# Kernel optimization log

Hardware: AMD Instinct MI355X
Metric: run time of the kernel (lower is better)

The kernel has to match this reference:

```python
import jax, jax.numpy as jnp
import numpy as np

D_MODEL = 512
EPS = 1e-5  # torch LayerNorm default


def _layernorm(x, g, b):
    mu = jnp.mean(x, axis=-1, keepdims=True)
    var = jnp.mean(jnp.square(x - mu), axis=-1, keepdims=True)
    return (x - mu) * jax.lax.rsqrt(var + EPS) * g + b


def setup_inputs() -> dict:
    key = jax.random.key(0)
    ks = jax.random.split(key, 12)
    d = D_MODEL
    s = 1.0 / np.sqrt(d)
    s4 = 1.0 / np.sqrt(4 * d)
    return {
        "x": jax.random.normal(ks[0], (4, 4096, d), dtype=jnp.float32),
        "Wq": jax.random.uniform(ks[1], (d, d), jnp.float32, -s, s),
        "bq": jax.random.uniform(ks[2], (d,), jnp.float32, -s, s),
        "Wk": jax.random.uniform(ks[3], (d, d), jnp.float32, -s, s),
        "bk": jax.random.uniform(ks[4], (d,), jnp.float32, -s, s),
        "Wv": jax.random.uniform(ks[5], (d, d), jnp.float32, -s, s),
        "bv": jax.random.uniform(ks[6], (d,), jnp.float32, -s, s),
        "g1": jnp.ones((d,), jnp.float32),
        "b1": jnp.zeros((d,), jnp.float32),
        "g2": jnp.ones((d,), jnp.float32),
        "b2": jnp.zeros((d,), jnp.float32),
        "W1": jax.random.uniform(ks[7], (d, 4 * d), jnp.float32, -s, s),
        "bf1": jax.random.uniform(ks[8], (4 * d,), jnp.float32, -s, s),
        "W2": jax.random.uniform(ks[9], (4 * d, d), jnp.float32, -s4, s4),
        "bf2": jax.random.uniform(ks[10], (d,), jnp.float32, -s4, s4),
    }


def reference(x, Wq, bq, Wk, bk, Wv, bv, g1, b1, g2, b2, W1, bf1, W2, bf2):
    # QKV projections: [b, s, d]
    Q = jnp.einsum("bsd,de->bse", x, Wq) + bq
    K = jnp.einsum("bsd,de->bse", x, Wk) + bk
    V = jnp.einsum("bsd,de->bse", x, Wv) + bv
    scale = 1.0 / jnp.sqrt(jnp.float32(K.shape[-1]))
    scores = jnp.einsum("bqd,bkd->bqk", Q, K) * scale  # [b, s, s]
    attn = jax.nn.softmax(scores, axis=-1)
    att = jnp.einsum("bqk,bkd->bqd", attn, V)
    x = _layernorm(x + att, g1, b1)
    h = jax.nn.relu(jnp.einsum("bsd,df->bsf", x, W1) + bf1)
    ffn = jnp.einsum("bsf,fd->bsd", h, W2) + bf2
    return _layernorm(x + ffn, g2, b2)
```

## Files before the change

### kernel.cpp

```cpp
#include <hip/hip_runtime.h>
#include <hip/hip_bf16.h>

typedef unsigned short u16;
typedef short bf16x8 __attribute__((ext_vector_type(8)));
typedef float f32x4 __attribute__((ext_vector_type(4)));

__device__ __forceinline__ float b2f(u16 u) {
  union { float f; unsigned int i; } v; v.i = ((unsigned int)u) << 16; return v.f;
}
__device__ __forceinline__ u16 f2b(float f) {
  union { float f; unsigned int i; } v; v.f = f;
  unsigned int r = v.i + 0x7fffu + ((v.i >> 16) & 1u);
  return (u16)(r >> 16);
}
__device__ __forceinline__ u16 to_b(float v) { return f2b(v); }
__device__ __forceinline__ u16 to_b(u16 v) { return v; }
__device__ __forceinline__ float to_f(float v) { return v; }
__device__ __forceinline__ float to_f(u16 v) { return b2f(v); }

__device__ __forceinline__ void gl_lds16(const u16* g, u16* l) {
  __builtin_amdgcn_global_load_lds(
      (const __attribute__((address_space(1))) unsigned int*)g,
      (__attribute__((address_space(3))) unsigned int*)l, 16, 0, 0);
}

template <bool RELU, bool ATOMIC>
__global__ __launch_bounds__(256)
void gemm_nt(const u16* __restrict__ A, const u16* __restrict__ Bt,
             const float* __restrict__ bias, void* __restrict__ Cv,
             int N, int K, int nsplit, int lda, int ldb, int ldc,
             long sA, long sB, long sC, float scale) {
  __shared__ __align__(16) u16 As[128 * 64];
  __shared__ __align__(16) u16 Bs[128 * 64];
  const int z = blockIdx.z;
  const int batch = z / nsplit, split = z - batch * nsplit;
  const int Ks = K / nsplit;
  const u16* Ab = A + (long)batch * sA + (long)split * Ks;
  const u16* Bb = Bt + (long)batch * sB + (long)split * Ks;
  const int m0 = blockIdx.y * 128, n0 = blockIdx.x * 128;
  const int t = threadIdx.x, w = t >> 6, lane = t & 63;
  const int wm = (w >> 1) * 64, wn = (w & 1) * 64;
  const int lr = lane & 15, q = lane >> 4;

  int srow[4], scol[4];
#pragma unroll
  for (int i = 0; i < 4; i++) {
    int n = w * 256 + i * 64 + lane;
    srow[i] = n >> 3;
    scol[i] = (((n & 7) ^ ((n >> 3) & 7)) * 8);
  }

  f32x4 acc[4][4];
#pragma unroll
  for (int i = 0; i < 4; i++)
#pragma unroll
    for (int j = 0; j < 4; j++) acc[i][j] = (f32x4){0.f, 0.f, 0.f, 0.f};

  for (int k0 = 0; k0 < Ks; k0 += 64) {
#pragma unroll
    for (int i = 0; i < 4; i++)
      gl_lds16(Ab + (long)(m0 + srow[i]) * lda + k0 + scol[i], &As[(w * 256 + i * 64) * 8]);
#pragma unroll
    for (int i = 0; i < 4; i++)
      gl_lds16(Bb + (long)(n0 + srow[i]) * ldb + k0 + scol[i], &Bs[(w * 256 + i * 64) * 8]);
    __syncthreads();
#pragma unroll
    for (int kk = 0; kk < 2; kk++) {
      bf16x8 af[4], bfr[4];
#pragma unroll
      for (int i = 0; i < 4; i++) {
        int row = wm + i * 16 + lr;
        af[i] = *(const bf16x8*)&As[row * 64 + (((kk * 4 + q) ^ (row & 7)) * 8)];
      }
#pragma unroll
      for (int j = 0; j < 4; j++) {
        int row = wn + j * 16 + lr;
        bfr[j] = *(const bf16x8*)&Bs[row * 64 + (((kk * 4 + q) ^ (row & 7)) * 8)];
      }
#pragma unroll
      for (int i = 0; i < 4; i++)
#pragma unroll
        for (int j = 0; j < 4; j++)
          acc[i][j] = __builtin_amdgcn_mfma_f32_16x16x32_bf16(af[i], bfr[j], acc[i][j], 0, 0, 0);
    }
    __syncthreads();
  }

#pragma unroll
  for (int j = 0; j < 4; j++) {
    int cg = n0 + wn + j * 16 + lr;
    float bb = (!ATOMIC && bias) ? bias[cg] : 0.0f;
#pragma unroll
    for (int i = 0; i < 4; i++) {
      int rbase = m0 + wm + i * 16 + q * 4;
#pragma unroll
      for (int r = 0; r < 4; r++) {
        float vv = acc[i][j][r] * scale;
        if (ATOMIC) {
          atomicAdd((float*)Cv + (long)batch * sC + (long)(rbase + r) * ldc + cg, vv);
        } else {
          vv += bb;
          if (RELU) vv = fmaxf(vv, 0.0f);
          ((u16*)Cv)[(long)batch * sC + (long)(rbase + r) * ldc + cg] = f2b(vv);
        }
      }
    }
  }
}

#define STAGE_K(kvv, kcc, sel)                                               \
  {                                                                          \
    _Pragma("unroll") for (int rr = 0; rr < 4; rr++)                         \
        gl_lds16(Kbase + (long)((kvv) * 128 + srow[rr]) * 1536 +             \
                     (kcc) * 128 + scol8[rr],                                \
                 &B2[(sel)][ldsd[rr]]);                                      \
  }
#define STAGE_V(kvv, dcc, sel)                                               \
  {                                                                          \
    _Pragma("unroll") for (int rr = 0; rr < 4; rr++)                         \
        gl_lds16(Vtb + (long)((dcc) * 128 + srow[rr]) * 4096 +               \
                     (kvv) * 128 + scol8[rr],                                \
                 &B2[(sel)][ldsd[rr]]);                                      \
  }
#define VMW4()  asm volatile("s_waitcnt vmcnt(4)" ::: "memory")
#define VMW0()  asm volatile("s_waitcnt vmcnt(0)" ::: "memory")
#define CFENCE() asm volatile("" ::: "memory")

__global__ __launch_bounds__(512, 2)
void flash_attn(const u16* __restrict__ QKV, const u16* __restrict__ Vt,
                u16* __restrict__ attp, float* __restrict__ lbp, float scl) {
  __shared__ __align__(16) u16 B2[2][128 * 128];
  __shared__ __align__(16) u16 Pb[128 * 136];
  const int flat = blockIdx.x;
  const int batch = (flat & 7) >> 1, half = flat & 1, qt = flat >> 3;
  const int t = threadIdx.x, w = t >> 6, lane = t & 63;
  const int lr = lane & 15, q = lane >> 4;
  const long rowbase = (long)batch * 4096 + qt * 128;
  const u16* Qrow  = QKV + (rowbase + w * 16 + lr) * 1536;
  const u16* Kbase = QKV + ((long)batch * 4096 + half * 2048) * 1536 + 512;
  const u16* Vtb   = Vt + (long)batch * 512 * 4096 + half * 2048;
  u16* Pw = &Pb[w * (16 * 136)];

  int srow[4], scol8[4], ldsd[4];
#pragma unroll
  for (int rr = 0; rr < 4; rr++) {
    int n = rr * 512 + t;
    srow[rr] = n >> 4;
    scol8[rr] = ((n & 15) ^ ((n >> 4) & 15)) * 8;
    ldsd[rr] = (rr * 512 + w * 64) * 8;
  }

  f32x4 O[32];
#pragma unroll
  for (int i = 0; i < 32; i++) O[i] = (f32x4){0.f, 0.f, 0.f, 0.f};
  float lsum[4] = {0.f, 0.f, 0.f, 0.f};

  STAGE_K(0, 0, 0);
  int par = 0;

  for (int kv = 0; kv < 16; kv++) {
    f32x4 S[8];
#pragma unroll
    for (int j = 0; j < 8; j++) S[j] = (f32x4){0.f, 0.f, 0.f, 0.f};

#pragma unroll
    for (int kc = 0; kc < 4; kc++) {
      if (kc < 3) { STAGE_K(kv, kc + 1, par ^ 1); }
      else        { STAGE_V(kv, 0, par ^ 1); }
      VMW4();
      __builtin_amdgcn_s_barrier();
      CFENCE();
      __builtin_amdgcn_s_setprio(1);
      bf16x8 Qf[4];
#pragma unroll
      for (int ss = 0; ss < 4; ss++)
        Qf[ss] = *(const bf16x8*)(Qrow + kc * 128 + ss * 32 + q * 8);
#pragma unroll
      for (int ss = 0; ss < 4; ss++)
#pragma unroll
        for (int j = 0; j < 8; j++) {
          int row = j * 16 + lr;
          bf16x8 Kf = *(const bf16x8*)&B2[par][row * 128 + (((ss * 4 + q) ^ lr) * 8)];
          S[j] = __builtin_amdgcn_mfma_f32_16x16x32_bf16(Qf[ss], Kf, S[j], 0, 0, 0);
        }
      __builtin_amdgcn_s_setprio(0);
      CFENCE();
      __builtin_amdgcn_s_barrier();
      par ^= 1;
    }

    float psum[4] = {0.f, 0.f, 0.f, 0.f};
#pragma unroll
    for (int j = 0; j < 8; j++)
#pragma unroll
      for (int r = 0; r < 4; r++) {
        float e = __expf(S[j][r] * scl);
        psum[r] += e;
        Pw[(q * 4 + r) * 136 + j * 16 + lr] = f2b(e);
      }
#pragma unroll
    for (int r = 0; r < 4; r++) {
#pragma unroll
      for (int o = 1; o < 16; o <<= 1) psum[r] += __shfl_xor(psum[r], o);
      lsum[r] += psum[r];
    }
    bf16x8 Pf[4];
#pragma unroll
    for (int t4 = 0; t4 < 4; t4++)
      Pf[t4] = *(const bf16x8*)&Pw[lr * 136 + t4 * 32 + q * 8];

#pragma unroll
    for (int dc = 0; dc < 4; dc++) {
      if (dc < 3) {
        STAGE_V(kv, dc + 1, par ^ 1);
        VMW4();
      } else if (kv < 15) {
        STAGE_K(kv + 1, 0, par ^ 1);
        VMW4();
      } else {
        VMW0();
      }
      __builtin_amdgcn_s_barrier();
      CFENCE();
      __builtin_amdgcn_s_setprio(1);
#pragma unroll
      for (int t4 = 0; t4 < 4; t4++)
#pragma unroll
        for (int j = 0; j < 8; j++) {
          int row = j * 16 + lr;
          bf16x8 Vf = *(const bf16x8*)&B2[par][row * 128 + (((t4 * 4 + q) ^ lr) * 8)];
          O[dc * 8 + j] = __builtin_amdgcn_mfma_f32_16x16x32_bf16(Pf[t4], Vf, O[dc * 8 + j], 0, 0, 0);
        }
      __builtin_amdgcn_s_setprio(0);
      CFENCE();
      __builtin_amdgcn_s_barrier();
      par ^= 1;
    }
  }

  u16* op = attp + (long)half * 16384 * 512;
#pragma unroll
  for (int i = 0; i < 32; i++) {
    int col = (i >> 3) * 128 + (i & 7) * 16 + lr;
#pragma unroll
    for (int r = 0; r < 4; r++)
      op[(rowbase + w * 16 + q * 4 + r) * 512 + col] = f2b(O[i][r]);
  }
  if (lr == 0)
#pragma unroll
    for (int r = 0; r < 4; r++)
      lbp[(long)half * 16384 + rowbase + w * 16 + q * 4 + r] = lsum[r];
}

template <typename TS>
__global__ __launch_bounds__(1024)
void transpose_b(const TS* __restrict__ src, u16* __restrict__ dst,
                 int R, int Cc, int src_ld, long sbs, long dbs) {
  __shared__ u16 tile[32][33];
  int r = blockIdx.y * 32 + threadIdx.y;
  int c = blockIdx.x * 32 + threadIdx.x;
  tile[threadIdx.y][threadIdx.x] = to_b(src[(long)blockIdx.z * sbs + (long)r * src_ld + c]);
  __syncthreads();
  int rr = blockIdx.x * 32 + threadIdx.y;
  int cc = blockIdx.y * 32 + threadIdx.x;
  dst[(long)blockIdx.z * dbs + (long)rr * R + cc] = tile[threadIdx.x][threadIdx.y];
}

__global__ __launch_bounds__(256)
void f32_to_bf16(const float* __restrict__ s, u16* __restrict__ d) {
  long i = ((long)blockIdx.x * 256 + threadIdx.x) * 8;
  float4 a0 = *(const float4*)(s + i);
  float4 a1 = *(const float4*)(s + i + 4);
  u16 tmp[8] = {f2b(a0.x), f2b(a0.y), f2b(a0.z), f2b(a0.w),
                f2b(a1.x), f2b(a1.y), f2b(a1.z), f2b(a1.w)};
  *(uint4*)(d + i) = *(uint4*)tmp;
}

__global__ __launch_bounds__(256)
void add_ln_att(const float* __restrict__ X, const u16* __restrict__ attp,
                const float* __restrict__ lbp,
                const float* __restrict__ g, const float* __restrict__ b,
                u16* __restrict__ O) {
  const int row = blockIdx.x * 4 + (threadIdx.x >> 6);
  const int lane = threadIdx.x & 63;
  const size_t base = (size_t)row * 512 + lane * 8;
  const float inv = 1.0f / (lbp[row] + lbp[16384 + row]);
  uint4 p0 = *(const uint4*)(attp + base);
  uint4 p1 = *(const uint4*)(attp + 16384L * 512 + base);
  const u16* s0 = (const u16*)&p0;
  const u16* s1 = (const u16*)&p1;
  float z[8];
  float s1a = 0.f, s2a = 0.f;
#pragma unroll
  for (int i = 0; i < 8; i++) {
    z[i] = X[base + i] + (b2f(s0[i]) + b2f(s1[i])) * inv;
    s1a += z[i]; s2a += z[i] * z[i];
  }
#pragma unroll
  for (int o = 32; o > 0; o >>= 1) { s1a += __shfl_xor(s1a, o); s2a += __shfl_xor(s2a, o); }
  const float mu = s1a * (1.0f / 512.0f);
  const float var = s2a * (1.0f / 512.0f) - mu * mu;
  const float rstd = rsqrtf(var + 1e-5f);
#pragma unroll
  for (int i = 0; i < 8; i++) {
    int c = lane * 8 + i;
    O[base + i] = f2b((z[i] - mu) * rstd * g[c] + b[c]);
  }
}

__global__ __launch_bounds__(256)
void add_ln_ffn(const u16* __restrict__ X, const u16* __restrict__ P0,
                const u16* __restrict__ P1, const float* __restrict__ eb,
                const float* __restrict__ g, const float* __restrict__ b,
                float* __restrict__ O) {
  const int row = blockIdx.x * 4 + (threadIdx.x >> 6);
  const int lane = threadIdx.x & 63;
  const size_t base = (size_t)row * 512 + lane * 8;
  uint4 xv = *(const uint4*)(X + base);
  uint4 a0 = *(const uint4*)(P0 + base);
  uint4 a1 = *(const uint4*)(P1 + base);
  const u16* xs = (const u16*)&xv;
  const u16* s0 = (const u16*)&a0;
  const u16* s1 = (const u16*)&a1;
  float z[8];
  float s1a = 0.f, s2a = 0.f;
#pragma unroll
  for (int i = 0; i < 8; i++) {
    int c = lane * 8 + i;
    z[i] = b2f(xs[i]) + b2f(s0[i]) + b2f(s1[i]) + eb[c];
    s1a += z[i]; s2a += z[i] * z[i];
  }
#pragma unroll
  for (int o = 32; o > 0; o >>= 1) { s1a += __shfl_xor(s1a, o); s2a += __shfl_xor(s2a, o); }
  const float mu = s1a * (1.0f / 512.0f);
  const float var = s2a * (1.0f / 512.0f) - mu * mu;
  const float rstd = rsqrtf(var + 1e-5f);
#pragma unroll
  for (int i = 0; i < 8; i++) {
    int c = lane * 8 + i;
    O[base + i] = (z[i] - mu) * rstd * g[c] + b[c];
  }
}

__global__ __launch_bounds__(256)
void concat3(const float* __restrict__ a, const float* __restrict__ b,
             const float* __restrict__ c, float* __restrict__ o) {
  int i = threadIdx.x + blockIdx.x * 256;
  if (i < 512) o[i] = a[i];
  else if (i < 1024) o[i] = b[i - 512];
  else if (i < 1536) o[i] = c[i - 1024];
}

extern "C" void kernel_launch(void* const* d_in, const int* in_sizes, int n_in,
                              void* d_out, int out_size, void* d_ws, size_t ws_size,
                              hipStream_t stream) {
  const float* x   = (const float*)d_in[0];
  const float* Wq  = (const float*)d_in[1];
  const float* bq  = (const float*)d_in[2];
  const float* Wk  = (const float*)d_in[3];
  const float* bk  = (const float*)d_in[4];
  const float* Wv  = (const float*)d_in[5];
  const float* bv  = (const float*)d_in[6];
  const float* g1  = (const float*)d_in[7];
  const float* b1  = (const float*)d_in[8];
  const float* g2  = (const float*)d_in[9];
  const float* b2  = (const float*)d_in[10];
  const float* W1  = (const float*)d_in[11];
  const float* bf1 = (const float*)d_in[12];
  const float* W2  = (const float*)d_in[13];
  const float* bf2 = (const float*)d_in[14];
  float* out = (float*)d_out;

  char* ws = (char*)d_ws;
  const size_t MB = 1048576;
  u16*   QKV   = (u16*)(ws + 0);
  u16*   Vt    = (u16*)(ws + 48 * MB);
  u16*   attp  = (u16*)(ws + 64 * MB);
  u16*   h     = (u16*)(ws + 64 * MB);
  float* lbp   = (float*)(ws + 128 * MB);
  u16*   x1    = (u16*)(ws + 129 * MB);
  u16*   ffnp  = (u16*)(ws + 145 * MB);
  u16*   xb    = (u16*)(ws + 145 * MB);
  u16*   wqkvt = (u16*)(ws + 177 * MB);
  u16*   w1t   = wqkvt + 1536 * 512;
  u16*   w2t   = w1t + 2048 * 512;
  float* bqkv  = (float*)(w2t + 512 * 2048);

  dim3 tb(32, 32);
  f32_to_bf16<<<4096, 256, 0, stream>>>(x, xb);
  transpose_b<float><<<dim3(16, 16, 1), tb, 0, stream>>>(Wq, wqkvt,              512, 512, 512, 0, 0);
  transpose_b<float><<<dim3(16, 16, 1), tb, 0, stream>>>(Wk, wqkvt + 512 * 512,  512, 512, 512, 0, 0);
  transpose_b<float><<<dim3(16, 16, 1), tb, 0, stream>>>(Wv, wqkvt + 1024 * 512, 512, 512, 512, 0, 0);
  transpose_b<float><<<dim3(64, 16, 1), tb, 0, stream>>>(W1, w1t, 512, 2048, 2048, 0, 0);
  transpose_b<float><<<dim3(16, 64, 1), tb, 0, stream>>>(W2, w2t, 2048, 512, 512, 0, 0);
  concat3<<<6, 256, 0, stream>>>(bq, bk, bv, bqkv);

  gemm_nt<false, false><<<dim3(12, 128, 1), 256, 0, stream>>>(
      xb, wqkvt, bqkv, QKV, 1536, 512, 1, 512, 512, 1536, 0, 0, 0, 1.0f);

  transpose_b<u16><<<dim3(16, 128, 4), tb, 0, stream>>>(
      QKV + 1024, Vt, 4096, 512, 1536, 4096L * 1536, 512L * 4096);

  const float scl = 0.044194173824159216f;
  flash_attn<<<dim3(256, 1, 1), 512, 0, stream>>>(QKV, Vt, attp, lbp, scl);

  add_ln_att<<<4096, 256, 0, stream>>>(x, attp, lbp, g1, b1, x1);
  gemm_nt<true, false><<<dim3(16, 128, 1), 256, 0, stream>>>(
      x1, w1t, bf1, h, 2048, 512, 1, 512, 512, 2048, 0, 0, 0, 1.0f);
  gemm_nt<false, false><<<dim3(4, 128, 2), 256, 0, stream>>>(
      h, w2t, nullptr, ffnp, 512, 1024, 1, 2048, 2048, 512,
      1024, 1024, 16384L * 512, 1.0f);
  add_ln_ffn<<<4096, 256, 0, stream>>>(
      x1, ffnp, ffnp + 16384L * 512, bf2, g2, b2, out);
}
```

Before: 522.1 us.

## Switch flash attention to 32x32x16 MFMA with shared-LDS P tile

The attention kernel moves from 16x16x32 to 32x32x16 bf16 MFMAs. Each wave now owns a 32-row query group and half of the KV or D columns, so operand loads from LDS are reused across a larger output tile. The whole-block P tile is written to LDS with a swizzle and read back after an extra barrier. Row sums are now reduced across 32 lanes and stored as four partials instead of two, and the add+LayerNorm kernel sums all four. The aim is fewer LDS reads per MFMA flop, at the cost of an extra barrier and a larger row-sum buffer.

After: 698.5 us. +33.8%, slower.

```diff
diff --git a/kernel.cpp b/kernel.cpp
--- a/kernel.cpp
+++ b/kernel.cpp
@@ -4,6 +4,7 @@
 typedef unsigned short u16;
 typedef short bf16x8 __attribute__((ext_vector_type(8)));
 typedef float f32x4 __attribute__((ext_vector_type(4)));
+typedef float f32x16 __attribute__((ext_vector_type(16)));
 
 __device__ __forceinline__ float b2f(u16 u) {
   union { float f; unsigned int i; } v; v.i = ((unsigned int)u) << 16; return v.f;
@@ -130,16 +131,16 @@
 void flash_attn(const u16* __restrict__ QKV, const u16* __restrict__ Vt,
                 u16* __restrict__ attp, float* __restrict__ lbp, float scl) {
   __shared__ __align__(16) u16 B2[2][128 * 128];
-  __shared__ __align__(16) u16 Pb[128 * 136];
+  __shared__ __align__(16) u16 Pb[128 * 128];
   const int flat = blockIdx.x;
   const int batch = (flat & 7) >> 1, half = flat & 1, qt = flat >> 3;
   const int t = threadIdx.x, w = t >> 6, lane = t & 63;
-  const int lr = lane & 15, q = lane >> 4;
+  const int rg = w & 3, sh = w >> 2;
+  const int c32 = lane & 31, hi = lane >> 5;
   const long rowbase = (long)batch * 4096 + qt * 128;
-  const u16* Qrow  = QKV + (rowbase + w * 16 + lr) * 1536;
+  const u16* Qp    = QKV + (rowbase + rg * 32 + c32) * 1536;
   const u16* Kbase = QKV + ((long)batch * 4096 + half * 2048) * 1536 + 512;
   const u16* Vtb   = Vt + (long)batch * 512 * 4096 + half * 2048;
-  u16* Pw = &Pb[w * (16 * 136)];
 
   int srow[4], scol8[4], ldsd[4];
 #pragma unroll
@@ -150,18 +151,24 @@
     ldsd[rr] = (rr * 512 + w * 64) * 8;
   }
 
-  f32x4 O[32];
-#pragma unroll
-  for (int i = 0; i < 32; i++) O[i] = (f32x4){0.f, 0.f, 0.f, 0.f};
-  float lsum[4] = {0.f, 0.f, 0.f, 0.f};
+  f32x16 O[8];
+#pragma unroll
+  for (int i = 0; i < 8; i++)
+#pragma unroll
+    for (int r = 0; r < 16; r++) O[i][r] = 0.f;
+  float lsum[16];
+#pragma unroll
+  for (int r = 0; r < 16; r++) lsum[r] = 0.f;
 
   STAGE_K(0, 0, 0);
   int par = 0;
 
   for (int kv = 0; kv < 16; kv++) {
-    f32x4 S[8];
-#pragma unroll
-    for (int j = 0; j < 8; j++) S[j] = (f32x4){0.f, 0.f, 0.f, 0.f};
+    f32x16 S[2];
+#pragma unroll
+    for (int tt = 0; tt < 2; tt++)
+#pragma unroll
+      for (int r = 0; r < 16; r++) S[tt][r] = 0.f;
 
 #pragma unroll
     for (int kc = 0; kc < 4; kc++) {
@@ -171,17 +178,17 @@
       __builtin_amdgcn_s_barrier();
       CFENCE();
       __builtin_amdgcn_s_setprio(1);
-      bf16x8 Qf[4];
-#pragma unroll
-      for (int ss = 0; ss < 4; ss++)
-        Qf[ss] = *(const bf16x8*)(Qrow + kc * 128 + ss * 32 + q * 8);
-#pragma unroll
-      for (int ss = 0; ss < 4; ss++)
-#pragma unroll
-        for (int j = 0; j < 8; j++) {
-          int row = j * 16 + lr;
-          bf16x8 Kf = *(const bf16x8*)&B2[par][row * 128 + (((ss * 4 + q) ^ lr) * 8)];
-          S[j] = __builtin_amdgcn_mfma_f32_16x16x32_bf16(Qf[ss], Kf, S[j], 0, 0, 0);
+      bf16x8 Qf[8];
+#pragma unroll
+      for (int ks = 0; ks < 8; ks++)
+        Qf[ks] = *(const bf16x8*)(Qp + kc * 128 + ks * 16 + hi * 8);
+#pragma unroll
+      for (int ks = 0; ks < 8; ks++)
+#pragma unroll
+        for (int tt = 0; tt < 2; tt++) {
+          int row = sh * 64 + tt * 32 + c32;
+          bf16x8 Kf = *(const bf16x8*)&B2[par][row * 128 + (((ks * 2 + hi) ^ (row & 15)) * 8)];
+          S[tt] = __builtin_amdgcn_mfma_f32_32x32x16_bf16(Qf[ks], Kf, S[tt], 0, 0, 0);
         }
       __builtin_amdgcn_s_setprio(0);
       CFENCE();
@@ -189,25 +196,24 @@
       par ^= 1;
     }
 
-    float psum[4] = {0.f, 0.f, 0.f, 0.f};
-#pragma unroll
-    for (int j = 0; j < 8; j++)
-#pragma unroll
-      for (int r = 0; r < 4; r++) {
-        float e = __expf(S[j][r] * scl);
-        psum[r] += e;
-        Pw[(q * 4 + r) * 136 + j * 16 + lr] = f2b(e);
+#pragma unroll
+    for (int tt = 0; tt < 2; tt++)
+#pragma unroll
+      for (int r = 0; r < 16; r++) {
+        float e = __expf(S[tt][r] * scl);
+        lsum[r] += e;
+        int qrow = rg * 32 + (r & 3) + 8 * (r >> 2) + 4 * hi;
+        int kvc = sh * 64 + tt * 32 + c32;
+        Pb[qrow * 128 + (((kvc >> 3) ^ (qrow & 15)) * 8) + (kvc & 7)] = f2b(e);
       }
-#pragma unroll
-    for (int r = 0; r < 4; r++) {
-#pragma unroll
-      for (int o = 1; o < 16; o <<= 1) psum[r] += __shfl_xor(psum[r], o);
-      lsum[r] += psum[r];
-    }
-    bf16x8 Pf[4];
-#pragma unroll
-    for (int t4 = 0; t4 < 4; t4++)
-      Pf[t4] = *(const bf16x8*)&Pw[lr * 136 + t4 * 32 + q * 8];
+    asm volatile("s_waitcnt lgkmcnt(0)" ::: "memory");
+    __builtin_amdgcn_s_barrier();
+    bf16x8 Pf[8];
+#pragma unroll
+    for (int ks = 0; ks < 8; ks++) {
+      int qrow = rg * 32 + c32;
+      Pf[ks] = *(const bf16x8*)&Pb[qrow * 128 + (((ks * 2 + hi) ^ (qrow & 15)) * 8)];
+    }
 
 #pragma unroll
     for (int dc = 0; dc < 4; dc++) {
@@ -224,12 +230,12 @@
       CFENCE();
       __builtin_amdgcn_s_setprio(1);
 #pragma unroll
-      for (int t4 = 0; t4 < 4; t4++)
-#pragma unroll
-        for (int j = 0; j < 8; j++) {
-          int row = j * 16 + lr;
-          bf16x8 Vf = *(const bf16x8*)&B2[par][row * 128 + (((t4 * 4 + q) ^ lr) * 8)];
-          O[dc * 8 + j] = __builtin_amdgcn_mfma_f32_16x16x32_bf16(Pf[t4], Vf, O[dc * 8 + j], 0, 0, 0);
+      for (int ks = 0; ks < 8; ks++)
+#pragma unroll
+        for (int i = 0; i < 2; i++) {
+          int drow = (sh + i * 2) * 32 + c32;
+          bf16x8 Vf = *(const bf16x8*)&B2[par][drow * 128 + (((ks * 2 + hi) ^ (drow & 15)) * 8)];
+          O[dc * 2 + i] = __builtin_amdgcn_mfma_f32_32x32x16_bf16(Pf[ks], Vf, O[dc * 2 + i], 0, 0, 0);
         }
       __builtin_amdgcn_s_setprio(0);
       CFENCE();
@@ -240,16 +246,24 @@
 
   u16* op = attp + (long)half * 16384 * 512;
 #pragma unroll
-  for (int i = 0; i < 32; i++) {
-    int col = (i >> 3) * 128 + (i & 7) * 16 + lr;
-#pragma unroll
-    for (int r = 0; r < 4; r++)
-      op[(rowbase + w * 16 + q * 4 + r) * 512 + col] = f2b(O[i][r]);
-  }
-  if (lr == 0)
-#pragma unroll
-    for (int r = 0; r < 4; r++)
-      lbp[(long)half * 16384 + rowbase + w * 16 + q * 4 + r] = lsum[r];
+  for (int o8 = 0; o8 < 8; o8++) {
+    int dcol = (o8 >> 1) * 128 + (sh + (o8 & 1) * 2) * 32 + c32;
+#pragma unroll
+    for (int r = 0; r < 16; r++) {
+      int qrow = rg * 32 + (r & 3) + 8 * (r >> 2) + 4 * hi;
+      op[(rowbase + qrow) * 512 + dcol] = f2b(O[o8][r]);
+    }
+  }
+#pragma unroll
+  for (int r = 0; r < 16; r++) {
+#pragma unroll
+    for (int o = 1; o < 32; o <<= 1) lsum[r] += __shfl_xor(lsum[r], o);
+  }
+  if (c32 < 16) {
+    int r = c32;
+    int qrow = rg * 32 + (r & 3) + 8 * (r >> 2) + 4 * hi;
+    lbp[(long)(half * 2 + sh) * 16384 + rowbase + qrow] = lsum[r];
+  }
 }
 
 template <typename TS>
@@ -284,7 +298,8 @@
   const int row = blockIdx.x * 4 + (threadIdx.x >> 6);
   const int lane = threadIdx.x & 63;
   const size_t base = (size_t)row * 512 + lane * 8;
-  const float inv = 1.0f / (lbp[row] + lbp[16384 + row]);
+  const float inv = 1.0f / (lbp[row] + lbp[16384 + row] +
+                            lbp[2 * 16384 + row] + lbp[3 * 16384 + row]);
   uint4 p0 = *(const uint4*)(attp + base);
   uint4 p1 = *(const uint4*)(attp + 16384L * 512 + base);
   const u16* s0 = (const u16*)&p0;
```
